# Optimization experiments

Measured on AMD Instinct MI355X. Metric: run time of the kernel, lower is better.

## Reference

```python
import jax, jax.numpy as jnp
import numpy as np

D_MODEL = 2048
N_HEADS = 16
HEAD_DIM = D_MODEL // N_HEADS


def setup_inputs() -> dict:
    key = jax.random.key(0)
    k_x, k_wqkv, k_bqkv, k_wo, k_bo = jax.random.split(key, 5)
    B, T = 4, 1024
    s_in = 1.0 / np.sqrt(D_MODEL)
    return {
        "x": jax.random.normal(k_x, (B, T, D_MODEL), dtype=jnp.float32),
        "w_qkv": jax.random.uniform(k_wqkv, (D_MODEL, 3 * D_MODEL), jnp.float32, -s_in, s_in),
        "b_qkv": jax.random.uniform(k_bqkv, (3 * D_MODEL,), jnp.float32, -s_in, s_in),
        "w_out": jax.random.uniform(k_wo, (D_MODEL, D_MODEL), jnp.float32, -s_in, s_in),
        "b_out": jax.random.uniform(k_bo, (D_MODEL,), jnp.float32, -s_in, s_in),
    }


def reference(x, w_qkv, b_qkv, w_out, b_out) -> jnp.ndarray:
    B, T, C = x.shape
    qkv = x @ w_qkv + b_qkv                      # [B, T, 3C]
    q, k, v = jnp.split(qkv, 3, axis=-1)
    # [B, H, T, Dh]
    q = q.reshape(B, T, N_HEADS, HEAD_DIM).transpose(0, 2, 1, 3)
    k = k.reshape(B, T, N_HEADS, HEAD_DIM).transpose(0, 2, 1, 3)
    v = v.reshape(B, T, N_HEADS, HEAD_DIM).transpose(0, 2, 1, 3)
    scale = 1.0 / np.sqrt(HEAD_DIM).astype(np.float32)
    att = jnp.einsum("bhqd,bhkd->bhqk", q, k) * scale   # [B, H, T, T]
    causal = jnp.tril(jnp.ones((T, T), dtype=bool))
    att = jnp.where(causal, att, -jnp.inf)
    att = jax.nn.softmax(att, axis=-1)
    out = jnp.einsum("bhqk,bhkd->bhqd", att, v)          # [B, H, T, Dh]
    out = out.transpose(0, 2, 1, 3).reshape(B, T, C)
    return out @ w_out + b_out
```

## Files before the change

kernel.cpp:

```cpp
#include <hip/hip_runtime.h>
#include <hip/hip_bf16.h>
#include <math.h>

#define DM    2048
#define DQKV  6144
#define NH    16
#define DH    128
#define TT    1024
#define BB    4

typedef __bf16 bf16_t;
typedef __bf16 bf16x4 __attribute__((ext_vector_type(4)));
typedef __bf16 bf16x8 __attribute__((ext_vector_type(8)));
typedef float  f32x4  __attribute__((ext_vector_type(4)));

__device__ __forceinline__ void async16(const void* g, void* lds) {
  __builtin_amdgcn_global_load_lds(
      (const __attribute__((address_space(1))) unsigned int*)g,
      (__attribute__((address_space(3))) unsigned int*)lds, 16, 0, 0);
}

__device__ __forceinline__ void block_barrier() {
  asm volatile("" ::: "memory");
  __builtin_amdgcn_s_barrier();
  asm volatile("" ::: "memory");
}

__global__ __launch_bounds__(256) void prep_kernel(
    const float* __restrict__ x, bf16_t* __restrict__ xb,
    const float* __restrict__ w_qkv, bf16_t* __restrict__ wqkv_t,
    const float* __restrict__ w_out, bf16_t* __restrict__ wout_t) {
  const int tid = threadIdx.x;
  const int bx = blockIdx.x;
  if (bx < 4096) {
    const size_t i = ((size_t)bx * 256 + tid) * 8;
    float4 a = *(const float4*)(x + i);
    float4 b = *(const float4*)(x + i + 4);
    bf16x8 o = {(bf16_t)a.x, (bf16_t)a.y, (bf16_t)a.z, (bf16_t)a.w,
                (bf16_t)b.x, (bf16_t)b.y, (bf16_t)b.z, (bf16_t)b.w};
    *(bf16x8*)(xb + i) = o;
    return;
  }
  __shared__ bf16_t tile[64][72];
  const float* W;
  bf16_t* Wt;
  int K, N, tn, tk;
  if (bx < 7168) {
    const int t = bx - 4096;
    W = w_qkv; Wt = wqkv_t; K = 2048; N = 6144;
    tn = (t % 96) * 64; tk = (t / 96) * 64;
  } else {
    const int t = bx - 7168;
    W = w_out; Wt = wout_t; K = 2048; N = 2048;
    tn = (t % 32) * 64; tk = (t / 32) * 64;
  }
  {
    int r = tid >> 2, c0 = (tid & 3) * 16;
    const float* src = W + (size_t)(tk + r) * N + tn + c0;
#pragma unroll
    for (int j = 0; j < 4; ++j) {
      float4 v = *(const float4*)(src + j * 4);
      bf16x4 t = {(bf16_t)v.x, (bf16_t)v.y, (bf16_t)v.z, (bf16_t)v.w};
      *(bf16x4*)&tile[r][c0 + j * 4] = t;
    }
  }
  __syncthreads();
  {
    int n = tid >> 2, c0 = (tid & 3) * 16;
    bf16_t* dst = Wt + (size_t)(tn + n) * K + tk + c0;
    bf16x8 t0 = {tile[c0 + 0][n], tile[c0 + 1][n], tile[c0 + 2][n],
                 tile[c0 + 3][n], tile[c0 + 4][n], tile[c0 + 5][n],
                 tile[c0 + 6][n], tile[c0 + 7][n]};
    bf16x8 t1 = {tile[c0 + 8][n],  tile[c0 + 9][n],  tile[c0 + 10][n],
                 tile[c0 + 11][n], tile[c0 + 12][n], tile[c0 + 13][n],
                 tile[c0 + 14][n], tile[c0 + 15][n]};
    *(bf16x8*)(dst) = t0;
    *(bf16x8*)(dst + 8) = t1;
  }
}

__global__ __launch_bounds__(256) void v_transpose_kernel(
    const bf16_t* __restrict__ qkv, bf16_t* __restrict__ Vt_g) {
  __shared__ bf16_t tile[64][72];
  const int tid = threadIdx.x;
  const int dt = blockIdx.x;
  const int tt = blockIdx.y;
  const int bh = blockIdx.z;
  const int b = bh >> 4, h = bh & 15;
  {
    int r = tid >> 2, c0 = (tid & 3) * 16;
    const bf16_t* src =
        qkv + (size_t)(b * TT + tt * 64 + r) * DQKV + 2 * DM + h * DH + dt * 64 + c0;
    *(bf16x8*)&tile[r][c0]     = *(const bf16x8*)(src);
    *(bf16x8*)&tile[r][c0 + 8] = *(const bf16x8*)(src + 8);
  }
  __syncthreads();
  {
    int n = tid >> 2, c0 = (tid & 3) * 16;
    bf16_t* dst = Vt_g + (size_t)(bh * DH + dt * 64 + n) * TT + tt * 64 + c0;
#pragma unroll
    for (int j = 0; j < 4; ++j) {
      bf16x4 t = {tile[c0 + j * 4 + 0][n], tile[c0 + j * 4 + 1][n],
                  tile[c0 + j * 4 + 2][n], tile[c0 + j * 4 + 3][n]};
      *(bf16x4*)(dst + j * 4) = t;
    }
  }
}

template <bool OUT_BF16, int BCH, bool WRITE_VT>
__global__ __launch_bounds__(512, 2) void gemm_big_kernel(
    const bf16_t* __restrict__ A, const bf16_t* __restrict__ Bt,
    const float* __restrict__ bias, void* __restrict__ out,
    bf16_t* __restrict__ vt, int M, int N, int K, int nbm) {
  __shared__ __align__(16) bf16_t As[2][256 * 64];
  __shared__ __align__(16) bf16_t Bs[2][BCH * 64 * 64];

  const int tid  = threadIdx.x;
  const int lane = tid & 63;
  const int wave = tid >> 6;
  const int ln   = lane & 15;
  const int quad = lane >> 4;

  const int cpx = gridDim.x >> 3;
  const int wg  = (blockIdx.x & 7) * cpx + (blockIdx.x >> 3);
  const int bm  = wg & (nbm - 1);
  const int bn  = wg / nbm;

  const bf16_t* Abase = A + (size_t)bm * 256 * K;
  const bf16_t* Bbase = Bt + (size_t)bn * (BCH * 64) * K;

  const int m0 = (wave >> 2) * 128;
  const int n0 = (wave & 3) * (BCH * 16);

  f32x4 acc[8][BCH] = {};

  const int NT = K >> 6;

  auto stageA = [&](int kt, int d) {
#pragma unroll
    for (int s = 0; s < 4; ++s) {
      const int fb  = s * 512 + wave * 64;
      const int f   = fb + lane;
      const int row = f >> 3, c = f & 7;
      const int gc  = c ^ (row & 7);
      async16(Abase + (size_t)row * K + kt * 64 + gc * 8,
              (char*)(&As[d][0]) + fb * 16);
    }
  };
  auto stageB = [&](int kt, int d) {
#pragma unroll
    for (int s = 0; s < BCH; ++s) {
      const int fb  = s * 512 + wave * 64;
      const int f   = fb + lane;
      const int row = f >> 3, c = f & 7;
      const int gc  = c ^ (row & 7);
      async16(Bbase + (size_t)row * K + kt * 64 + gc * 8,
              (char*)(&Bs[d][0]) + fb * 16);
    }
  };
  auto vm_lpt = [&] {
    if constexpr (BCH == 3)
      asm volatile("s_waitcnt vmcnt(7)" ::: "memory");
    else
      asm volatile("s_waitcnt vmcnt(6)" ::: "memory");
  };

  stageA(0, 0);
  stageB(0, 0);
  stageA(1, 1);
  stageB(1, 1);
  vm_lpt();
  block_barrier();

  for (int kt = 0; kt < NT; ++kt) {
    const int cur = kt & 1;

    bf16x8 af[8][2], bfr[BCH][2];
#pragma unroll
    for (int ks = 0; ks < 2; ++ks) {
#pragma unroll
      for (int i = 0; i < 8; ++i) {
        const int row = m0 + 16 * i + ln;
        const int c = (ks * 4 + quad) ^ (row & 7);
        af[i][ks] =
            *(const bf16x8*)((const char*)(&As[cur][0]) + ((row * 8 + c) << 4));
      }
#pragma unroll
      for (int j = 0; j < BCH; ++j) {
        const int row = n0 + 16 * j + ln;
        const int c = (ks * 4 + quad) ^ (row & 7);
        bfr[j][ks] =
            *(const bf16x8*)((const char*)(&Bs[cur][0]) + ((row * 8 + c) << 4));
      }
    }
    asm volatile("s_waitcnt lgkmcnt(0)" ::: "memory");
    block_barrier();

    if (kt + 2 < NT) stageA(kt + 2, cur);
    __builtin_amdgcn_s_setprio(1);
#pragma unroll
    for (int i = 0; i < 8; ++i)
#pragma unroll
      for (int j = 0; j < BCH; ++j)
        acc[i][j] = __builtin_amdgcn_mfma_f32_16x16x32_bf16(af[i][0], bfr[j][0],
                                                            acc[i][j], 0, 0, 0);
    __builtin_amdgcn_s_setprio(0);
    if (kt + 2 < NT) stageB(kt + 2, cur);
    __builtin_amdgcn_s_setprio(1);
#pragma unroll
    for (int i = 0; i < 8; ++i)
#pragma unroll
      for (int j = 0; j < BCH; ++j)
        acc[i][j] = __builtin_amdgcn_mfma_f32_16x16x32_bf16(af[i][1], bfr[j][1],
                                                            acc[i][j], 0, 0, 0);
    __builtin_amdgcn_s_setprio(0);

    if (kt + 2 < NT)
      vm_lpt();
    else
      asm volatile("s_waitcnt vmcnt(0)" ::: "memory");
    block_barrier();
  }

#pragma unroll
  for (int i = 0; i < 8; ++i) {
    const int rowg = bm * 256 + m0 + 16 * i + quad * 4;
#pragma unroll
    for (int j = 0; j < BCH; ++j) {
      const int cb   = bn * (BCH * 64) + n0 + 16 * j;
      const int colg = cb + ln;
      const float bb = bias[colg];
      if (WRITE_VT && cb >= 2 * DM) {
        const int vrow = ((rowg >> 10) << 11) + (colg - 2 * DM);
        bf16x4 v = {(bf16_t)(acc[i][j][0] + bb), (bf16_t)(acc[i][j][1] + bb),
                    (bf16_t)(acc[i][j][2] + bb), (bf16_t)(acc[i][j][3] + bb)};
        *(bf16x4*)(vt + (size_t)vrow * TT + (rowg & (TT - 1))) = v;
      } else {
#pragma unroll
        for (int r = 0; r < 4; ++r) {
          float val = acc[i][j][r] + bb;
          if (OUT_BF16)
            ((bf16_t*)out)[(size_t)(rowg + r) * N + colg] = (bf16_t)val;
          else
            ((float*)out)[(size_t)(rowg + r) * N + colg] = val;
        }
      }
    }
  }
}

__global__ __launch_bounds__(256, 2) void gemm128_kernel(
    const bf16_t* __restrict__ A, const bf16_t* __restrict__ Bt,
    const float* __restrict__ bias, float* __restrict__ out,
    int M, int N, int K, int nbm) {
  __shared__ __align__(16) bf16_t As[2][128 * 64];
  __shared__ __align__(16) bf16_t Bs[2][128 * 64];

  const int tid  = threadIdx.x;
  const int lane = tid & 63;
  const int wave = tid >> 6;
  const int ln   = lane & 15;
  const int quad = lane >> 4;

  const int cpx = gridDim.x >> 3;
  const int wg  = (blockIdx.x & 7) * cpx + (blockIdx.x >> 3);
  const int bm  = wg & (nbm - 1);
  const int bn  = wg / nbm;

  const bf16_t* Abase = A + (size_t)bm * 128 * K;
  const bf16_t* Bbase = Bt + (size_t)bn * 128 * K;

  const int m0 = (wave >> 1) * 64;
  const int n0 = (wave & 1) * 64;

  f32x4 acc[4][4] = {};

  const int NT = K >> 6;

  auto stageA = [&](int kt, int d) {
#pragma unroll
    for (int s = 0; s < 4; ++s) {
      const int fb  = s * 256 + wave * 64;
      const int f   = fb + lane;
      const int row = f >> 3, c = f & 7;
      const int gc  = c ^ (row & 7);
      async16(Abase + (size_t)row * K + kt * 64 + gc * 8,
              (char*)(&As[d][0]) + fb * 16);
    }
  };
  auto stageB = [&](int kt, int d) {
#pragma unroll
    for (int s = 0; s < 4; ++s) {
      const int fb  = s * 256 + wave * 64;
      const int f   = fb + lane;
      const int row = f >> 3, c = f & 7;
      const int gc  = c ^ (row & 7);
      async16(Bbase + (size_t)row * K + kt * 64 + gc * 8,
              (char*)(&Bs[d][0]) + fb * 16);
    }
  };

  stageA(0, 0);
  stageB(0, 0);
  stageA(1, 1);
  stageB(1, 1);
  asm volatile("s_waitcnt vmcnt(8)" ::: "memory");
  block_barrier();

  for (int kt = 0; kt < NT; ++kt) {
    const int cur = kt & 1;

    bf16x8 af[4][2], bfr[4][2];
#pragma unroll
    for (int ks = 0; ks < 2; ++ks) {
#pragma unroll
      for (int i = 0; i < 4; ++i) {
        const int row = m0 + 16 * i + ln;
        const int c = (ks * 4 + quad) ^ (row & 7);
        af[i][ks] =
            *(const bf16x8*)((const char*)(&As[cur][0]) + ((row * 8 + c) << 4));
      }
#pragma unroll
      for (int j = 0; j < 4; ++j) {
        const int row = n0 + 16 * j + ln;
        const int c = (ks * 4 + quad) ^ (row & 7);
        bfr[j][ks] =
            *(const bf16x8*)((const char*)(&Bs[cur][0]) + ((row * 8 + c) << 4));
      }
    }
    asm volatile("s_waitcnt lgkmcnt(0)" ::: "memory");
    block_barrier();

    if (kt + 2 < NT) stageA(kt + 2, cur);
    __builtin_amdgcn_s_setprio(1);
#pragma unroll
    for (int i = 0; i < 4; ++i)
#pragma unroll
      for (int j = 0; j < 4; ++j)
        acc[i][j] = __builtin_amdgcn_mfma_f32_16x16x32_bf16(af[i][0], bfr[j][0],
                                                            acc[i][j], 0, 0, 0);
    __builtin_amdgcn_s_setprio(0);
    if (kt + 2 < NT) stageB(kt + 2, cur);
    __builtin_amdgcn_s_setprio(1);
#pragma unroll
    for (int i = 0; i < 4; ++i)
#pragma unroll
      for (int j = 0; j < 4; ++j)
        acc[i][j] = __builtin_amdgcn_mfma_f32_16x16x32_bf16(af[i][1], bfr[j][1],
                                                            acc[i][j], 0, 0, 0);
    __builtin_amdgcn_s_setprio(0);

    if (kt + 2 < NT)
      asm volatile("s_waitcnt vmcnt(8)" ::: "memory");
    else
      asm volatile("s_waitcnt vmcnt(0)" ::: "memory");
    block_barrier();
  }

#pragma unroll
  for (int i = 0; i < 4; ++i) {
    const int rowg = bm * 128 + m0 + 16 * i + quad * 4;
#pragma unroll
    for (int j = 0; j < 4; ++j) {
      const int colg = bn * 128 + n0 + 16 * j + ln;
      const float bb = bias[colg];
#pragma unroll
      for (int r = 0; r < 4; ++r)
        out[(size_t)(rowg + r) * N + colg] = acc[i][j][r] + bb;
    }
  }
}

__global__ __launch_bounds__(256, 2) void attn_kernel(
    const bf16_t* __restrict__ qkv, const bf16_t* __restrict__ Vt_g,
    bf16_t* __restrict__ attout) {
  const int bx = blockIdx.x;
  const int bh = bx & 63;
  const int j_  = bx >> 6;
  const int rr  = j_ >> 2, cc_ = j_ & 3;
  const int qt  = (rr & 1) ? (rr * 4 + (3 - cc_)) : (rr * 4 + cc_);
  const int b  = bh >> 4;
  const int h  = bh & 15;
  const int tid  = threadIdx.x;
  const int lane = tid & 63;
  const int wave = tid >> 6;
  const int ln   = lane & 15;
  const int quad = lane >> 4;

  __shared__ __align__(16) bf16_t Ks[2][64 * 128];
  __shared__ __align__(16) bf16_t Vs[2][128 * 64];
  __shared__ __align__(16) bf16_t Ps[4 * 16 * 64];

  const float scale = 0.08838834764831845f;
  const float SHIFT = 12.0f;
  const int q0 = qt * 64 + wave * 16;

  bf16x8 aq[4];
  {
    const bf16_t* qrow = qkv + (size_t)(b * TT + q0 + ln) * DQKV + h * DH;
#pragma unroll
    for (int kt = 0; kt < 4; ++kt)
      aq[kt] = *(const bf16x8*)(qrow + kt * 32 + quad * 8);
  }

  auto stage = [&](int c, int buf) {
    const int kc = c * 64;
#pragma unroll
    for (int j = 0; j < 4; ++j) {
      const int fb = j * 256 + wave * 64;
      const int l  = fb + lane;
      {
        const int row = l >> 4, cc = l & 15;
        const int gc  = cc ^ (row & 7);
        const bf16_t* g =
            qkv + (size_t)(b * TT + kc + row) * DQKV + DM + h * DH + gc * 8;
        async16(g, (char*)(&Ks[buf][0]) + fb * 16);
      }
      {
        const int d = l >> 3, cc = l & 7;
        const int gc = cc ^ (d & 7);
        const bf16_t* g = Vt_g + (size_t)(bh * DH + d) * TT + kc + gc * 8;
        async16(g, (char*)(&Vs[buf][0]) + fb * 16);
      }
    }
  };

  f32x4 o[8] = {};
  float lp[4] = {0.f, 0.f, 0.f, 0.f};

  stage(0, 0);

  for (int c = 0; c <= qt; ++c) {
    const int cur = c & 1;
    const char* Kc = (const char*)(&Ks[cur][0]);
    const char* Vc = (const char*)(&Vs[cur][0]);

    asm volatile("s_waitcnt lgkmcnt(0)" ::: "memory");
    block_barrier();
    if (c < qt) {
      stage(c + 1, cur ^ 1);
      asm volatile("s_waitcnt vmcnt(8)" ::: "memory");
    } else {
      asm volatile("s_waitcnt vmcnt(0)" ::: "memory");
    }
    block_barrier();

    f32x4 sacc[4];
    __builtin_amdgcn_s_setprio(1);
#pragma unroll
    for (int jt = 0; jt < 4; ++jt) {
      sacc[jt] = (f32x4){0.f, 0.f, 0.f, 0.f};
#pragma unroll
      for (int kt = 0; kt < 4; ++kt) {
        const int row = jt * 16 + ln;
        const int sc  = (kt * 4 + quad) ^ (row & 7);
        bf16x8 bk = *(const bf16x8*)(Kc + row * 256 + sc * 16);
        sacc[jt] = __builtin_amdgcn_mfma_f32_16x16x32_bf16(aq[kt], bk,
                                                           sacc[jt], 0, 0, 0);
      }
    }
    __builtin_amdgcn_s_setprio(0);

    const int kc = c * 64;
    const bool diag = (c == qt);
#pragma unroll
    for (int jt = 0; jt < 4; ++jt) {
      const int colg = kc + jt * 16 + ln;
#pragma unroll
      for (int r = 0; r < 4; ++r) {
        float sv = sacc[jt][r] * scale - SHIFT;
        if (diag && colg > q0 + quad * 4 + r) sv = -1e30f;
        float pv = __expf(sv);
        lp[r] += pv;
        const int row = quad * 4 + r;
        const int col = jt * 16 + ln;
        const int sc  = (col >> 3) ^ (row & 7);
        Ps[wave * 1024 + row * 64 + sc * 8 + (col & 7)] = (bf16_t)pv;
      }
    }

    __builtin_amdgcn_s_setprio(1);
#pragma unroll
    for (int ks = 0; ks < 2; ++ks) {
      const int psc = (ks * 4 + quad) ^ (ln & 7);
      bf16x8 ap =
          *(const bf16x8*)((const char*)Ps + wave * 2048 + ln * 128 + psc * 16);
#pragma unroll
      for (int nt = 0; nt < 8; ++nt) {
        const int row = nt * 16 + ln;
        const int sc  = (ks * 4 + quad) ^ (row & 7);
        bf16x8 bv = *(const bf16x8*)(Vc + row * 128 + sc * 16);
        o[nt] = __builtin_amdgcn_mfma_f32_16x16x32_bf16(ap, bv, o[nt], 0, 0, 0);
      }
    }
    __builtin_amdgcn_s_setprio(0);
  }

#pragma unroll
  for (int off = 1; off < 16; off <<= 1)
#pragma unroll
    for (int r = 0; r < 4; ++r) lp[r] += __shfl_xor(lp[r], off, 64);

#pragma unroll
  for (int r = 0; r < 4; ++r) {
    float inv = 1.0f / lp[r];
    int t = q0 + quad * 4 + r;
    bf16_t* orow = attout + (size_t)(b * TT + t) * DM + h * DH;
#pragma unroll
    for (int nt = 0; nt < 8; ++nt)
      orow[nt * 16 + ln] = (bf16_t)(o[nt][r] * inv);
  }
}

extern "C" void kernel_launch(void* const* d_in, const int* in_sizes, int n_in,
                              void* d_out, int out_size, void* d_ws,
                              size_t ws_size, hipStream_t stream) {
  const float* x     = (const float*)d_in[0];
  const float* w_qkv = (const float*)d_in[1];
  const float* b_qkv = (const float*)d_in[2];
  const float* w_out = (const float*)d_in[3];
  const float* b_out = (const float*)d_in[4];
  float* out = (float*)d_out;

  char* ws = (char*)d_ws;
  bf16_t* qkv    = (bf16_t*)(ws);
  bf16_t* wqkv_t = (bf16_t*)(ws + 50331648);
  bf16_t* wout_t = (bf16_t*)(ws + 75497472);
  bf16_t* xb     = (bf16_t*)(ws + 83886080);
  bf16_t* attout = xb;

  const bool fuse_vt = (ws_size >= 117440512);
  bf16_t* Vt_g = fuse_vt ? (bf16_t*)(ws + 100663296) : wqkv_t;

  prep_kernel<<<dim3(8192), dim3(256), 0, stream>>>(x, xb, w_qkv, wqkv_t,
                                                    w_out, wout_t);
  if (fuse_vt) {
    gemm_big_kernel<true, 3, true><<<dim3(512), dim3(512), 0, stream>>>(
        xb, wqkv_t, b_qkv, qkv, Vt_g, 4096, 6144, 2048, 16);
  } else {
    gemm_big_kernel<true, 3, false><<<dim3(512), dim3(512), 0, stream>>>(
        xb, wqkv_t, b_qkv, qkv, nullptr, 4096, 6144, 2048, 16);
    v_transpose_kernel<<<dim3(2, 16, 64), dim3(256), 0, stream>>>(qkv, Vt_g);
  }
  attn_kernel<<<dim3(1024), dim3(256), 0, stream>>>(qkv, Vt_g, attout);
  gemm128_kernel<<<dim3(512), dim3(256), 0, stream>>>(
      attout, wout_t, b_out, out, 4096, 2048, 2048, 32);
}
```

Before: 318.8 us.

## Split GEMM main loop into four phases with finer-grained staged prefetch

Restructures the bf16 GEMM K-loop into four sub-phases (two row halves times two k-halves), loading fewer A/B fragments at a time. Global-to-LDS prefetch of the next tiles is interleaved at chunk granularity across the phases, with matching vmcnt waits. This cuts register pressure from the fragment arrays and spreads memory traffic across MFMA work. The cost is many more block barriers per iteration and a more fragile ordering of async loads against LDS reuse.

```diff
diff --git a/kernel.cpp b/kernel.cpp
--- a/kernel.cpp
+++ b/kernel.cpp
@@ -136,87 +136,132 @@
 
   const int NT = K >> 6;
 
-  auto stageA = [&](int kt, int d) {
-#pragma unroll
-    for (int s = 0; s < 4; ++s) {
-      const int fb  = s * 512 + wave * 64;
-      const int f   = fb + lane;
-      const int row = f >> 3, c = f & 7;
-      const int gc  = c ^ (row & 7);
-      async16(Abase + (size_t)row * K + kt * 64 + gc * 8,
-              (char*)(&As[d][0]) + fb * 16);
-    }
+  auto sA = [&](int kt, int d, int s) {
+    const int fb  = s * 512 + wave * 64;
+    const int f   = fb + lane;
+    const int row = f >> 3, c = f & 7;
+    const int gc  = c ^ (row & 7);
+    async16(Abase + (size_t)row * K + kt * 64 + gc * 8,
+            (char*)(&As[d][0]) + fb * 16);
   };
-  auto stageB = [&](int kt, int d) {
-#pragma unroll
-    for (int s = 0; s < BCH; ++s) {
-      const int fb  = s * 512 + wave * 64;
-      const int f   = fb + lane;
-      const int row = f >> 3, c = f & 7;
-      const int gc  = c ^ (row & 7);
-      async16(Bbase + (size_t)row * K + kt * 64 + gc * 8,
-              (char*)(&Bs[d][0]) + fb * 16);
-    }
+  auto sB = [&](int kt, int d, int s) {
+    const int fb  = s * 512 + wave * 64;
+    const int f   = fb + lane;
+    const int row = f >> 3, c = f & 7;
+    const int gc  = c ^ (row & 7);
+    async16(Bbase + (size_t)row * K + kt * 64 + gc * 8,
+            (char*)(&Bs[d][0]) + fb * 16);
   };
-  auto vm_lpt = [&] {
-    if constexpr (BCH == 3)
-      asm volatile("s_waitcnt vmcnt(7)" ::: "memory");
-    else
-      asm volatile("s_waitcnt vmcnt(6)" ::: "memory");
-  };
-
-  stageA(0, 0);
-  stageB(0, 0);
-  stageA(1, 1);
-  stageB(1, 1);
-  vm_lpt();
+
+#pragma unroll
+  for (int s = 0; s < 4; ++s) sA(0, 0, s);
+#pragma unroll
+  for (int s = 0; s < BCH; ++s) sB(0, 0, s);
+  sA(1, 1, 0);
+  sA(1, 1, 2);
+  asm volatile("s_waitcnt vmcnt(2)" ::: "memory");
   block_barrier();
 
   for (int kt = 0; kt < NT; ++kt) {
     const int cur = kt & 1;
-
-    bf16x8 af[8][2], bfr[BCH][2];
-#pragma unroll
-    for (int ks = 0; ks < 2; ++ks) {
-#pragma unroll
-      for (int i = 0; i < 8; ++i) {
-        const int row = m0 + 16 * i + ln;
-        const int c = (ks * 4 + quad) ^ (row & 7);
-        af[i][ks] =
-            *(const bf16x8*)((const char*)(&As[cur][0]) + ((row * 8 + c) << 4));
-      }
-#pragma unroll
-      for (int j = 0; j < BCH; ++j) {
-        const int row = n0 + 16 * j + ln;
-        const int c = (ks * 4 + quad) ^ (row & 7);
-        bfr[j][ks] =
-            *(const bf16x8*)((const char*)(&Bs[cur][0]) + ((row * 8 + c) << 4));
-      }
-    }
+    const char* cA = (const char*)(&As[cur][0]);
+    const char* cB = (const char*)(&Bs[cur][0]);
+    bf16x8 a[4], b[BCH];
+
+#pragma unroll
+    for (int i = 0; i < 4; ++i) {
+      const int row = m0 + 16 * i + ln;
+      const int c = quad ^ (row & 7);
+      a[i] = *(const bf16x8*)(cA + ((row * 8 + c) << 4));
+    }
+#pragma unroll
+    for (int j = 0; j < BCH; ++j) {
+      const int row = n0 + 16 * j + ln;
+      const int c = quad ^ (row & 7);
+      b[j] = *(const bf16x8*)(cB + ((row * 8 + c) << 4));
+    }
+    if (kt + 1 < NT) {
+      sA(kt + 1, cur ^ 1, 1);
+      sA(kt + 1, cur ^ 1, 3);
+#pragma unroll
+      for (int s = 0; s < BCH; ++s) sB(kt + 1, cur ^ 1, s);
+    }
+    block_barrier();
     asm volatile("s_waitcnt lgkmcnt(0)" ::: "memory");
-    block_barrier();
-
-    if (kt + 2 < NT) stageA(kt + 2, cur);
-    __builtin_amdgcn_s_setprio(1);
-#pragma unroll
-    for (int i = 0; i < 8; ++i)
+    __builtin_amdgcn_s_setprio(1);
+#pragma unroll
+    for (int i = 0; i < 4; ++i)
 #pragma unroll
       for (int j = 0; j < BCH; ++j)
-        acc[i][j] = __builtin_amdgcn_mfma_f32_16x16x32_bf16(af[i][0], bfr[j][0],
+        acc[i][j] = __builtin_amdgcn_mfma_f32_16x16x32_bf16(a[i], b[j],
                                                             acc[i][j], 0, 0, 0);
     __builtin_amdgcn_s_setprio(0);
-    if (kt + 2 < NT) stageB(kt + 2, cur);
-    __builtin_amdgcn_s_setprio(1);
-#pragma unroll
-    for (int i = 0; i < 8; ++i)
+    block_barrier();
+
+#pragma unroll
+    for (int i = 0; i < 4; ++i) {
+      const int row = m0 + 64 + 16 * i + ln;
+      const int c = quad ^ (row & 7);
+      a[i] = *(const bf16x8*)(cA + ((row * 8 + c) << 4));
+    }
+    block_barrier();
+    asm volatile("s_waitcnt lgkmcnt(0)" ::: "memory");
+    __builtin_amdgcn_s_setprio(1);
+#pragma unroll
+    for (int i = 0; i < 4; ++i)
 #pragma unroll
       for (int j = 0; j < BCH; ++j)
-        acc[i][j] = __builtin_amdgcn_mfma_f32_16x16x32_bf16(af[i][1], bfr[j][1],
+        acc[4 + i][j] = __builtin_amdgcn_mfma_f32_16x16x32_bf16(
+            a[i], b[j], acc[4 + i][j], 0, 0, 0);
+    __builtin_amdgcn_s_setprio(0);
+    block_barrier();
+
+#pragma unroll
+    for (int i = 0; i < 4; ++i) {
+      const int row = m0 + 16 * i + ln;
+      const int c = (4 + quad) ^ (row & 7);
+      a[i] = *(const bf16x8*)(cA + ((row * 8 + c) << 4));
+    }
+#pragma unroll
+    for (int j = 0; j < BCH; ++j) {
+      const int row = n0 + 16 * j + ln;
+      const int c = (4 + quad) ^ (row & 7);
+      b[j] = *(const bf16x8*)(cB + ((row * 8 + c) << 4));
+    }
+    block_barrier();
+    asm volatile("s_waitcnt lgkmcnt(0)" ::: "memory");
+    __builtin_amdgcn_s_setprio(1);
+#pragma unroll
+    for (int i = 0; i < 4; ++i)
+#pragma unroll
+      for (int j = 0; j < BCH; ++j)
+        acc[i][j] = __builtin_amdgcn_mfma_f32_16x16x32_bf16(a[i], b[j],
                                                             acc[i][j], 0, 0, 0);
     __builtin_amdgcn_s_setprio(0);
-
+    block_barrier();
+
+#pragma unroll
+    for (int i = 0; i < 4; ++i) {
+      const int row = m0 + 64 + 16 * i + ln;
+      const int c = (4 + quad) ^ (row & 7);
+      a[i] = *(const bf16x8*)(cA + ((row * 8 + c) << 4));
+    }
+    if (kt + 2 < NT) {
+      sA(kt + 2, cur, 0);
+      sA(kt + 2, cur, 2);
+    }
+    block_barrier();
+    asm volatile("s_waitcnt lgkmcnt(0)" ::: "memory");
+    __builtin_amdgcn_s_setprio(1);
+#pragma unroll
+    for (int i = 0; i < 4; ++i)
+#pragma unroll
+      for (int j = 0; j < BCH; ++j)
+        acc[4 + i][j] = __builtin_amdgcn_mfma_f32_16x16x32_bf16(
+            a[i], b[j], acc[4 + i][j], 0, 0, 0);
+    __builtin_amdgcn_s_setprio(0);
     if (kt + 2 < NT)
-      vm_lpt();
+      asm volatile("s_waitcnt vmcnt(2)" ::: "memory");
     else
       asm volatile("s_waitcnt vmcnt(0)" ::: "memory");
     block_barrier();
```

New measurement: 333.9 us. 1.05x slower.
